# Kernel optimization log

Measured on AMD Instinct MI355X. Metric: run time of the kernel, lower is better.

Reference implementation:

```python
import jax, jax.numpy as jnp
import numpy as np

T, B, D, H = 512, 64, 512, 512

def setup_inputs() -> dict:
    key = jax.random.key(0)
    ks = jax.random.split(key, 14)
    s = 0.02
    inp = {
        "inputs": jax.random.normal(ks[0], (T, B, D), dtype=jnp.float32),
        # gate linears: weight [D+H, H] (transposed torch layout), bias [H]
        "Wf": jax.random.normal(ks[1], (D + H, H), dtype=jnp.float32) * s,
        "bf": jax.random.normal(ks[2], (H,), dtype=jnp.float32) * s,
        "Wi": jax.random.normal(ks[3], (D + H, H), dtype=jnp.float32) * s,
        "bi": jax.random.normal(ks[4], (H,), dtype=jnp.float32) * s,
        "Wg": jax.random.normal(ks[5], (D + H, H), dtype=jnp.float32) * s,
        "bg": jax.random.normal(ks[6], (H,), dtype=jnp.float32) * s,
        "Wo": jax.random.normal(ks[7], (D + H, H), dtype=jnp.float32) * s,
        "bo": jax.random.normal(ks[8], (H,), dtype=jnp.float32) * s,
        # residual linears on hidden state: [H, H], no bias
        "Rf": jax.random.normal(ks[9], (H, H), dtype=jnp.float32) * s,
        "Ri": jax.random.normal(ks[10], (H, H), dtype=jnp.float32) * s,
        "Rg": jax.random.normal(ks[11], (H, H), dtype=jnp.float32) * s,
        "Ro": jax.random.normal(ks[12], (H, H), dtype=jnp.float32) * s,
    }
    return inp


def reference(inputs, Wf, bf, Wi, bi, Wg, bg, Wo, bo, Rf, Ri, Rg, Ro):
    # QLSTM forward (eval mode, gate_dropout inactive). states=None -> zeros.
    batch = inputs.shape[1]
    hidden = Wf.shape[1]
    h0 = jnp.zeros((batch, hidden), dtype=inputs.dtype)
    c0 = jnp.zeros((batch, hidden), dtype=inputs.dtype)

    # Fuse the 4 gate GEMMs into one [D+H, 4H] matmul and the 4 residual
    # GEMMs into one [H, 4H] matmul (same math, fewer launches).
    W4 = jnp.concatenate([Wf, Wi, Wg, Wo], axis=1)   # [D+H, 4H]
    b4 = jnp.concatenate([bf, bi, bg, bo], axis=0)   # [4H]
    R4 = jnp.concatenate([Rf, Ri, Rg, Ro], axis=1)   # [H, 4H]

    def step(carry, x):
        hx, cx = carry
        combined = jnp.concatenate([x, hx], axis=1)            # [B, D+H]
        z = combined @ W4 + b4 + hx @ R4                        # [B, 4H]
        f, i, g, o = jnp.split(z, 4, axis=1)
        f = jax.nn.sigmoid(f)
        i = jax.nn.sigmoid(i)
        g = jnp.tanh(g)
        o = jax.nn.sigmoid(o)
        cx = f * cx + i * g
        hx = o * jnp.tanh(cx)
        return (hx, cx), hx

    (hx, cx), stacked = jax.lax.scan(step, (h0, c0), inputs)
    return stacked, hx, cx
```

## Files before the change

kernel.cpp:

```cpp
#include <hip/hip_runtime.h>
#include <hip/hip_bf16.h>

typedef __attribute__((ext_vector_type(8))) short s16x8;
typedef __attribute__((ext_vector_type(4))) float f32x4;

__device__ __forceinline__ ushort f2bf(float x) {
  __hip_bfloat16 b = __float2bfloat16(x);
  return *reinterpret_cast<ushort*>(&b);
}
__device__ __forceinline__ float bf2f(ushort u) {
  union { unsigned int i; float f; } c; c.i = ((unsigned int)u) << 16; return c.f;
}
__device__ __forceinline__ float sigm_fast(float z) {
  return __builtin_amdgcn_rcpf(1.0f + __builtin_amdgcn_exp2f(z * -1.44269504088896f));
}

__global__ __launch_bounds__(256) void pack_weights(
    const float* __restrict__ Wf, const float* __restrict__ Wi,
    const float* __restrict__ Wg, const float* __restrict__ Wo,
    const float* __restrict__ Rf, const float* __restrict__ Ri,
    const float* __restrict__ Rg, const float* __restrict__ Ro,
    const float* __restrict__ bfp, const float* __restrict__ bip,
    const float* __restrict__ bgp, const float* __restrict__ bop,
    ushort* __restrict__ Wx, ushort* __restrict__ Rs, float* __restrict__ bp)
{
  const int p = blockIdx.x * 8 + (threadIdx.x >> 5);
  const int kk = (threadIdx.x & 31) * 16;
  const int gate = p & 3;
  const int hcol = (p >> 5) * 8 + ((p >> 4) & 1) * 4 + ((p & 15) >> 2);
  const float* W = (gate == 0) ? Wf : (gate == 1) ? Wi : (gate == 2) ? Wg : Wo;
  const float* R = (gate == 0) ? Rf : (gate == 1) ? Ri : (gate == 2) ? Rg : Ro;
  union { ushort u[16]; s16x8 v[2]; } wb, rb;
#pragma unroll
  for (int e = 0; e < 16; ++e) {
    const int k = kk + e;
    wb.u[e] = f2bf(W[(size_t)k * 512 + hcol]);
    rb.u[e] = f2bf(W[(size_t)(512 + k) * 512 + hcol] + R[(size_t)k * 512 + hcol]);
  }
  *(s16x8*)(Wx + (size_t)p * 512 + kk)     = wb.v[0];
  *(s16x8*)(Wx + (size_t)p * 512 + kk + 8) = wb.v[1];
  *(s16x8*)(Rs + (size_t)p * 512 + kk)     = rb.v[0];
  *(s16x8*)(Rs + (size_t)p * 512 + kk + 8) = rb.v[1];
  if ((threadIdx.x & 31) == 0) {
    const float* B = (gate == 0) ? bfp : (gate == 1) ? bip : (gate == 2) ? bgp : bop;
    bp[p] = B[hcol];
  }
}

__global__ __launch_bounds__(512, 1) void fused_kernel(
    const float* __restrict__ x, const ushort* __restrict__ Wx,
    const ushort* __restrict__ Rs, const float* __restrict__ bp,
    const ushort* __restrict__ zxr, ushort* __restrict__ zxw,
    ushort* __restrict__ hbuf, float* __restrict__ csave,
    int* __restrict__ flags, ushort* __restrict__ hsave,
    float* __restrict__ cfinal, int t0, int CH, int zxt0, int do_rec)
{
  __shared__ ushort lds_u[33280];
  const int tid = threadIdx.x;
  const int wid = tid >> 6;
  const int lane = tid & 63;
  const int l15 = lane & 15;
  const int hi = lane >> 4;

  if (blockIdx.x >= 32) {
    if (zxt0 >= 512) return;
    const int zbid = blockIdx.x - 32;
    const int pg = zbid & 15;
    const int ts = zbid >> 4;
    const int mpair = wid >> 2;
    const int np = wid & 3;
    const int q = pg * 4 + np;
    s16x8 Bg[2][16];
#pragma unroll
    for (int nt = 0; nt < 2; ++nt)
#pragma unroll
      for (int kc = 0; kc < 16; ++kc)
        Bg[nt][kc] = *(const s16x8*)(Wx + (size_t)(q * 32 + nt * 16 + l15) * 512 + kc * 32 + hi * 8);
    const int tper = CH >> 3;
    for (int tt = 0; tt < tper; ++tt) {
      const int tl = ts * tper + tt;
      const int t = zxt0 + tl;
      const float4* x4 = (const float4*)(x + (size_t)t * 32768);
#pragma unroll
      for (int j = 0; j < 16; ++j) {
        const int i4 = j * 512 + tid;
        const float4 v = x4[i4];
        const int row = i4 >> 7;
        const int c0 = (i4 & 127) * 4;
        ushort4 u;
        u.x = f2bf(v.x); u.y = f2bf(v.y); u.z = f2bf(v.z); u.w = f2bf(v.w);
        *(ushort4*)(&lds_u[row * 520 + c0]) = u;
      }
      __syncthreads();
#pragma unroll
      for (int a = 0; a < 2; ++a) {
        const int mt = mpair * 2 + a;
        f32x4 a0 = {0.f, 0.f, 0.f, 0.f};
        f32x4 a1 = {0.f, 0.f, 0.f, 0.f};
#pragma unroll
        for (int kc = 0; kc < 16; ++kc) {
          const s16x8 af = *(const s16x8*)(&lds_u[(mt * 16 + l15) * 520 + kc * 32 + hi * 8]);
          a0 = __builtin_amdgcn_mfma_f32_16x16x32_bf16(af, Bg[0][kc], a0, 0, 0, 0);
          a1 = __builtin_amdgcn_mfma_f32_16x16x32_bf16(af, Bg[1][kc], a1, 0, 0, 0);
        }
        union { ushort u[8]; s16x8 v; } ub;
#pragma unroll
        for (int r = 0; r < 4; ++r) { ub.u[r] = f2bf(a0[r]); ub.u[4 + r] = f2bf(a1[r]); }
        *(s16x8*)(zxw + ((((size_t)tl * 4 + mt) * 64 + q) * 64 + lane) * 8) = ub.v;
      }
      __syncthreads();
    }
    return;
  }

  if (!do_rec) return;
  ushort* hsl = lds_u;
  ushort* tbuf = lds_u + 8192;
  const int bid = blockIdx.x;
  const int g = bid >> 3;
  const int mem = bid & 7;
  const int q = mem * 8 + wid;
  const int gate = lane & 3;

  f32x4 Brg[2][16];
#pragma unroll
  for (int nt = 0; nt < 2; ++nt)
#pragma unroll
    for (int kc = 0; kc < 16; ++kc) {
      Brg[nt][kc] = *(const f32x4*)(Rs + (size_t)(q * 32 + nt * 16 + l15) * 512 + kc * 32 + hi * 8);
      asm volatile("" : "+v"(Brg[nt][kc]));
    }
  const float b0 = bp[q * 32 + l15];
  const float b1 = bp[q * 32 + 16 + l15];

  float cst[2][4];
  float* csp = csave + ((size_t)(bid * 8 + wid) * 64 + lane) * 8;
  if (t0 == 0) {
#pragma unroll
    for (int i = 0; i < 2; ++i)
#pragma unroll
      for (int r = 0; r < 4; ++r) cst[i][r] = 0.0f;
  } else {
#pragma unroll
    for (int i = 0; i < 2; ++i)
#pragma unroll
      for (int r = 0; r < 4; ++r) cst[i][r] = csp[i * 4 + r];
  }

  const int srow = hi * 4 + gate;
  const int hcol0 = q * 8 + (l15 >> 2);
  const int crow = tid >> 5;
  const int cbyte = (tid & 31) * 32;
  const int cswz = (crow & 7) << 4;
  const int srcofs = crow * 512 + (cbyte >> 1);
  const int wofs0 = (crow * 1024 + (cbyte ^ cswz)) >> 1;
  const int wofs1 = (crow * 1024 + ((cbyte + 16) ^ cswz)) >> 1;
  const int abase = l15 * 1024 + hi * 16;
  const int aswz = (l15 & 7) << 4;
  int* const myflag = &flags[(g * 8 + mem) * 16];
  const int pollofs = (g * 8 + (lane & 7)) * 16;

  for (int tl = 0; tl < CH; ++tl) {
    const int t = t0 + tl;
    if (tl > 0) {
      asm volatile("s_waitcnt vmcnt(0)" ::: "memory");
      __syncthreads();
      if (tid == 0)
        __hip_atomic_store(myflag, t, __ATOMIC_RELAXED, __HIP_MEMORY_SCOPE_AGENT);
    }
    const s16x8 zv = *(const s16x8*)(zxr + ((((size_t)tl * 4 + g) * 64 + q) * 64 + lane) * 8);
    if (tl > 0) {
      int v;
      do {
        v = __hip_atomic_load(&flags[pollofs], __ATOMIC_RELAXED, __HIP_MEMORY_SCOPE_AGENT);
      } while (!__all(v >= t));
      asm volatile("" ::: "memory");
    }
    const ushort* hs = hbuf + ((size_t)tl * 4 + g) * 8192;
    const s16x8 h0 = *(const s16x8*)(hs + srcofs);
    const s16x8 h1 = *(const s16x8*)(hs + srcofs + 8);
    *(s16x8*)(&hsl[wofs0]) = h0;
    *(s16x8*)(&hsl[wofs1]) = h1;
    __syncthreads();
    f32x4 a0 = {0.f, 0.f, 0.f, 0.f};
    f32x4 a1 = {0.f, 0.f, 0.f, 0.f};
#pragma unroll
    for (int kc = 0; kc < 16; ++kc) {
      const s16x8 af = *(const s16x8*)(&hsl[((abase + kc * 64) ^ aswz) >> 1]);
      a0 = __builtin_amdgcn_mfma_f32_16x16x32_bf16(af, __builtin_bit_cast(s16x8, Brg[0][kc]), a0, 0, 0, 0);
      a1 = __builtin_amdgcn_mfma_f32_16x16x32_bf16(af, __builtin_bit_cast(s16x8, Brg[1][kc]), a1, 0, 0, 0);
    }
    float hv[2], cv[2];
#pragma unroll
    for (int nt = 0; nt < 2; ++nt) {
      float hr[4];
#pragma unroll
      for (int r = 0; r < 4; ++r) {
        float z = (nt ? a1[r] : a0[r]) + bf2f((ushort)zv[nt * 4 + r]) + (nt ? b1 : b0);
        const float zz = (gate == 2) ? z + z : z;
        const float s = sigm_fast(zz);
        const float act = (gate == 2) ? (s + s - 1.0f) : s;
        const int ai = __float_as_int(act);
        const float fv = __int_as_float(__builtin_amdgcn_mov_dpp(ai, 0x00, 0xF, 0xF, true));
        const float iv = __int_as_float(__builtin_amdgcn_mov_dpp(ai, 0x55, 0xF, 0xF, true));
        const float gv = __int_as_float(__builtin_amdgcn_mov_dpp(ai, 0xAA, 0xF, 0xF, true));
        const float ov = __int_as_float(__builtin_amdgcn_mov_dpp(ai, 0xFF, 0xF, 0xF, true));
        const float cn = fmaf(fv, cst[nt][r], iv * gv);
        cst[nt][r] = cn;
        const float s2 = sigm_fast(cn + cn);
        hr[r] = ov * (s2 + s2 - 1.0f);
      }
      hv[nt] = (gate == 0) ? hr[0] : (gate == 1) ? hr[1] : (gate == 2) ? hr[2] : hr[3];
      cv[nt] = (gate == 0) ? cst[nt][0] : (gate == 1) ? cst[nt][1]
             : (gate == 2) ? cst[nt][2] : cst[nt][3];
    }
    const ushort pb0 = f2bf(hv[0]), pb1 = f2bf(hv[1]);
    tbuf[wid * 128 + srow * 8 + (l15 >> 2)]     = pb0;
    tbuf[wid * 128 + srow * 8 + (l15 >> 2) + 4] = pb1;
    asm volatile("s_waitcnt lgkmcnt(0)" ::: "memory");
    __builtin_amdgcn_sched_barrier(0);
    if (tl != CH - 1) {
      if (lane < 16) {
        const unsigned long long* rp = (const unsigned long long*)&tbuf[wid * 128 + lane * 8];
        ushort* dst = hbuf + ((size_t)(tl + 1) * 4 + g) * 8192 + lane * 512 + q * 8;
        __hip_atomic_store((unsigned long long*)dst, rp[0],
                           __ATOMIC_RELAXED, __HIP_MEMORY_SCOPE_AGENT);
        __hip_atomic_store((unsigned long long*)(dst + 4), rp[1],
                           __ATOMIC_RELAXED, __HIP_MEMORY_SCOPE_AGENT);
      }
    } else {
      ushort* hn0 = hbuf + (size_t)g * 8192;
      hn0[srow * 512 + hcol0]     = pb0;
      hn0[srow * 512 + hcol0 + 4] = pb1;
    }
    ushort2 hp; hp.x = pb0; hp.y = pb1;
    *(ushort2*)(hsave + (((size_t)t * 4 + g) * 8 + mem) * 1024 + wid * 128 + lane * 2) = hp;
    if (t == 511) {
      float* cf = cfinal + (((size_t)(g * 8 + mem) * 8 + wid) * 64 + lane) * 2;
      cf[0] = cv[0]; cf[1] = cv[1];
    }
  }
#pragma unroll
  for (int i = 0; i < 2; ++i)
#pragma unroll
    for (int r = 0; r < 4; ++r) csp[i * 4 + r] = cst[i][r];
}

__global__ __launch_bounds__(256) void reorder_kernel(
    const ushort* __restrict__ hsave, const float* __restrict__ cfinal,
    float* __restrict__ dout)
{
  __shared__ ushort lds[8192];
  const int t = blockIdx.x;
  const int g = blockIdx.y;
  const int tid = threadIdx.x;
  const s16x8* src = (const s16x8*)(hsave + ((size_t)t * 4 + g) * 8192);
#pragma unroll
  for (int j = 0; j < 4; ++j) {
    const int i = j * 256 + tid;
    *(s16x8*)(&lds[i * 8]) = src[i];
  }
  __syncthreads();
  const int srow = tid >> 4;
  const int cb = (tid & 15) * 32;
  float buf[32];
#pragma unroll
  for (int cc = 0; cc < 32; ++cc) {
    const int col = cb + cc;
    const int q = col >> 3;
    const int memb = q >> 3;
    const int wd = q & 7;
    const int nt = (col >> 2) & 1;
    const int l15v = ((col & 3) << 2) | (srow & 3);
    const int lanev = ((srow >> 2) << 4) | l15v;
    buf[cc] = bf2f(lds[memb * 1024 + wd * 128 + lanev * 2 + nt]);
  }
  float* o = dout + (size_t)t * 32768 + (size_t)(g * 16 + srow) * 512 + cb;
#pragma unroll
  for (int j = 0; j < 8; ++j) *(float4*)(o + j * 4) = *(const float4*)(&buf[j * 4]);
  if (t == 511) {
    float* oh = dout + (size_t)16777216 + (size_t)(g * 16 + srow) * 512 + cb;
#pragma unroll
    for (int j = 0; j < 8; ++j) *(float4*)(oh + j * 4) = *(const float4*)(&buf[j * 4]);
    float cbuf[32];
#pragma unroll
    for (int cc = 0; cc < 32; ++cc) {
      const int col = cb + cc;
      const int q = col >> 3;
      const int memb = q >> 3;
      const int wd = q & 7;
      const int nt = (col >> 2) & 1;
      const int l15v = ((col & 3) << 2) | (srow & 3);
      const int lanev = ((srow >> 2) << 4) | l15v;
      cbuf[cc] = cfinal[(((size_t)(g * 8 + memb) * 8 + wd) * 64 + lanev) * 2 + nt];
    }
    float* oc = dout + (size_t)16809984 + (size_t)(g * 16 + srow) * 512 + cb;
#pragma unroll
    for (int j = 0; j < 8; ++j) *(float4*)(oc + j * 4) = *(const float4*)(&cbuf[j * 4]);
  }
}

extern "C" void kernel_launch(void* const* d_in, const int* in_sizes, int n_in,
                              void* d_out, int out_size, void* d_ws, size_t ws_size,
                              hipStream_t stream)
{
  const float* x   = (const float*)d_in[0];
  const float* Wf  = (const float*)d_in[1];
  const float* bfp = (const float*)d_in[2];
  const float* Wi  = (const float*)d_in[3];
  const float* bip = (const float*)d_in[4];
  const float* Wg  = (const float*)d_in[5];
  const float* bgp = (const float*)d_in[6];
  const float* Wo  = (const float*)d_in[7];
  const float* bop = (const float*)d_in[8];
  const float* Rf  = (const float*)d_in[9];
  const float* Ri  = (const float*)d_in[10];
  const float* Rg  = (const float*)d_in[11];
  const float* Ro  = (const float*)d_in[12];
  float* dout = (float*)d_out;
  char* ws = (char*)d_ws;

  const size_t o_Wx = 0;
  const size_t o_Rs = 2097152;
  const size_t o_bp = 4194304;
  const size_t o_z0 = o_bp + 8192;

  int CH = 64;
  for (;;) {
    const size_t need = o_z0 + 2 * (size_t)CH * 262144 + (size_t)(CH + 1) * 65536
                      + 524288 + 2048 + 33554432 + 131072;
    if (need <= ws_size || CH <= 8) break;
    CH >>= 1;
  }
  const size_t zsz  = (size_t)CH * 262144;
  const size_t o_z1 = o_z0 + zsz;
  const size_t o_hb = o_z1 + zsz;
  const size_t o_cs = o_hb + (size_t)(CH + 1) * 65536;
  const size_t o_fl = o_cs + 524288;
  const size_t o_hs = o_fl + 2048;
  const size_t o_cf = o_hs + 33554432;

  ushort* Wx   = (ushort*)(ws + o_Wx);
  ushort* Rs   = (ushort*)(ws + o_Rs);
  float*  bp   = (float*)(ws + o_bp);
  ushort* zx0  = (ushort*)(ws + o_z0);
  ushort* zx1  = (ushort*)(ws + o_z1);
  ushort* hb   = (ushort*)(ws + o_hb);
  float*  csv  = (float*)(ws + o_cs);
  int*    fl   = (int*)(ws + o_fl);
  ushort* hsv  = (ushort*)(ws + o_hs);
  float*  cfin = (float*)(ws + o_cf);

  pack_weights<<<256, 256, 0, stream>>>(Wf, Wi, Wg, Wo, Rf, Ri, Rg, Ro,
                                        bfp, bip, bgp, bop, Wx, Rs, bp);
  hipMemsetAsync(hb, 0, 65536, stream);
  hipMemsetAsync(fl, 0, 2048, stream);

  fused_kernel<<<160, 512, 0, stream>>>(x, Wx, Rs, bp, zx1, zx0, hb, csv, fl,
                                        hsv, cfin, 0, CH, 0, 0);
  const int nch = 512 / CH;
  for (int c = 0; c < nch; ++c) {
    const ushort* zr = (c & 1) ? zx1 : zx0;
    ushort* zw       = (c & 1) ? zx0 : zx1;
    fused_kernel<<<160, 512, 0, stream>>>(x, Wx, Rs, bp, zr, zw, hb, csv, fl,
                                          hsv, cfin, c * CH, CH, (c + 1) * CH, 1);
  }
  reorder_kernel<<<dim3(512, 4), 256, 0, stream>>>(hsv, cfin, dout);
}
```

Baseline: 1.722 ms.

## Replace flag-based step barrier with timestamp-tagged packed hidden-state words

Removes the per-step flag store, flag polling and vmcnt drain. Each 64-bit word now carries three bf16 hidden values plus a 16-bit step tag. Consumers spin on the tags of the data they need, and the loads for the next step and the zx values are issued early. This cuts one round trip of cross-block synchronisation on the recurrent critical path. In exchange it packs three values per 8 bytes, which adds traffic overhead, adds a block barrier before publishing, and depends on relaxed-atomic 64-bit stores being seen whole.

```diff
diff --git a/kernel.cpp b/kernel.cpp
--- a/kernel.cpp
+++ b/kernel.cpp
@@ -3,6 +3,7 @@
 
 typedef __attribute__((ext_vector_type(8))) short s16x8;
 typedef __attribute__((ext_vector_type(4))) float f32x4;
+typedef unsigned long long u64;
 
 __device__ __forceinline__ ushort f2bf(float x) {
   __hip_bfloat16 b = __float2bfloat16(x);
@@ -13,6 +14,9 @@
 }
 __device__ __forceinline__ float sigm_fast(float z) {
   return __builtin_amdgcn_rcpf(1.0f + __builtin_amdgcn_exp2f(z * -1.44269504088896f));
+}
+__device__ __forceinline__ u64 aload(const u64* p) {
+  return __hip_atomic_load(p, __ATOMIC_RELAXED, __HIP_MEMORY_SCOPE_AGENT);
 }
 
 __global__ __launch_bounds__(256) void pack_weights(
@@ -51,9 +55,9 @@
     const float* __restrict__ x, const ushort* __restrict__ Wx,
     const ushort* __restrict__ Rs, const float* __restrict__ bp,
     const ushort* __restrict__ zxr, ushort* __restrict__ zxw,
-    ushort* __restrict__ hbuf, float* __restrict__ csave,
-    int* __restrict__ flags, ushort* __restrict__ hsave,
-    float* __restrict__ cfinal, int t0, int CH, int zxt0, int do_rec)
+    u64* __restrict__ hbc, float* __restrict__ csave,
+    ushort* __restrict__ hsave, float* __restrict__ cfinal,
+    int t0, int CH, int zxt0, int do_rec)
 {
   __shared__ ushort lds_u[33280];
   const int tid = threadIdx.x;
@@ -148,39 +152,54 @@
   }
 
   const int srow = hi * 4 + gate;
-  const int hcol0 = q * 8 + (l15 >> 2);
   const int crow = tid >> 5;
+  const int c0 = (tid & 31) * 16;
+  const int memr = c0 >> 6;
+  const int q0c = (crow * 4 + ((c0 & 63) >> 4)) * 6;
   const int cbyte = (tid & 31) * 32;
   const int cswz = (crow & 7) << 4;
-  const int srcofs = crow * 512 + (cbyte >> 1);
   const int wofs0 = (crow * 1024 + (cbyte ^ cswz)) >> 1;
   const int wofs1 = (crow * 1024 + ((cbyte + 16) ^ cswz)) >> 1;
   const int abase = l15 * 1024 + hi * 16;
   const int aswz = (l15 & 7) << 4;
-  int* const myflag = &flags[(g * 8 + mem) * 16];
-  const int pollofs = (g * 8 + (lane & 7)) * 16;
+  const int prow = tid / 24;
+  const int pspan = (tid / 6) & 3;
+  const int pk = tid - (tid / 6) * 6;
+  const int mc0p = pspan * 16 + pk * 3;
+  const int tb0 = (((mc0p) >> 3) & 7) * 128 + prow * 8 + (mc0p & 7);
+  const int mc1p = (mc0p + 1 < (pspan + 1) * 16) ? mc0p + 1 : mc0p;
+  const int mc2p = (mc0p + 2 < (pspan + 1) * 16) ? mc0p + 2 : mc0p;
+  const int tb1 = ((mc1p >> 3) & 7) * 128 + prow * 8 + (mc1p & 7);
+  const int tb2 = ((mc2p >> 3) & 7) * 128 + prow * 8 + (mc2p & 7);
+
+  u64 chv[6];
+  {
+    const u64* cb = hbc + (((size_t)0 * 4 + g) * 8 + memr) * 384 + q0c;
+#pragma unroll
+    for (int i = 0; i < 6; ++i) chv[i] = aload(cb + i);
+  }
+  s16x8 zv = *(const s16x8*)(zxr + ((((size_t)0 * 4 + g) * 64 + q) * 64 + lane) * 8);
 
   for (int tl = 0; tl < CH; ++tl) {
     const int t = t0 + tl;
-    if (tl > 0) {
-      asm volatile("s_waitcnt vmcnt(0)" ::: "memory");
-      __syncthreads();
-      if (tid == 0)
-        __hip_atomic_store(myflag, t, __ATOMIC_RELAXED, __HIP_MEMORY_SCOPE_AGENT);
-    }
-    const s16x8 zv = *(const s16x8*)(zxr + ((((size_t)tl * 4 + g) * 64 + q) * 64 + lane) * 8);
-    if (tl > 0) {
-      int v;
-      do {
-        v = __hip_atomic_load(&flags[pollofs], __ATOMIC_RELAXED, __HIP_MEMORY_SCOPE_AGENT);
-      } while (!__all(v >= t));
-      asm volatile("" ::: "memory");
-    }
-    const ushort* hs = hbuf + ((size_t)tl * 4 + g) * 8192;
-    const s16x8 h0 = *(const s16x8*)(hs + srcofs);
-    const s16x8 h1 = *(const s16x8*)(hs + srcofs + 8);
-    *(s16x8*)(&hsl[wofs0]) = h0;
-    *(s16x8*)(&hsl[wofs1]) = h1;
+    const ushort tau = (ushort)t;
+    {
+      const u64* vb = hbc + (((size_t)tl * 4 + g) * 8 + memr) * 384 + q0c;
+      for (;;) {
+        int ok = 1;
+#pragma unroll
+        for (int i = 0; i < 6; ++i)
+          if ((ushort)(chv[i] >> 48) != tau) { chv[i] = aload(vb + i); ok = 0; }
+        if (ok) break;
+      }
+    }
+    union { ushort u[8]; s16x8 v; } ha, hb2;
+#pragma unroll
+    for (int j = 0; j < 8; ++j)  ha.u[j]      = (ushort)(chv[j / 3] >> (16 * (j % 3)));
+#pragma unroll
+    for (int j = 8; j < 16; ++j) hb2.u[j - 8] = (ushort)(chv[j / 3] >> (16 * (j % 3)));
+    *(s16x8*)(&hsl[wofs0]) = ha.v;
+    *(s16x8*)(&hsl[wofs1]) = hb2.v;
     __syncthreads();
     f32x4 a0 = {0.f, 0.f, 0.f, 0.f};
     f32x4 a1 = {0.f, 0.f, 0.f, 0.f};
@@ -217,27 +236,30 @@
     const ushort pb0 = f2bf(hv[0]), pb1 = f2bf(hv[1]);
     tbuf[wid * 128 + srow * 8 + (l15 >> 2)]     = pb0;
     tbuf[wid * 128 + srow * 8 + (l15 >> 2) + 4] = pb1;
-    asm volatile("s_waitcnt lgkmcnt(0)" ::: "memory");
-    __builtin_amdgcn_sched_barrier(0);
-    if (tl != CH - 1) {
-      if (lane < 16) {
-        const unsigned long long* rp = (const unsigned long long*)&tbuf[wid * 128 + lane * 8];
-        ushort* dst = hbuf + ((size_t)(tl + 1) * 4 + g) * 8192 + lane * 512 + q * 8;
-        __hip_atomic_store((unsigned long long*)dst, rp[0],
-                           __ATOMIC_RELAXED, __HIP_MEMORY_SCOPE_AGENT);
-        __hip_atomic_store((unsigned long long*)(dst + 4), rp[1],
-                           __ATOMIC_RELAXED, __HIP_MEMORY_SCOPE_AGENT);
-      }
-    } else {
-      ushort* hn0 = hbuf + (size_t)g * 8192;
-      hn0[srow * 512 + hcol0]     = pb0;
-      hn0[srow * 512 + hcol0 + 4] = pb1;
-    }
-    ushort2 hp; hp.x = pb0; hp.y = pb1;
-    *(ushort2*)(hsave + (((size_t)t * 4 + g) * 8 + mem) * 1024 + wid * 128 + lane * 2) = hp;
-    if (t == 511) {
-      float* cf = cfinal + (((size_t)(g * 8 + mem) * 8 + wid) * 64 + lane) * 2;
-      cf[0] = cv[0]; cf[1] = cv[1];
+    if (tl + 1 < CH) {
+      const u64* nb = hbc + (((size_t)(tl + 1) * 4 + g) * 8 + memr) * 384 + q0c;
+#pragma unroll
+      for (int i = 0; i < 6; ++i) chv[i] = aload(nb + i);
+      zv = *(const s16x8*)(zxr + ((((size_t)(tl + 1) * 4 + g) * 64 + q) * 64 + lane) * 8);
+    }
+    {
+      ushort2 hp; hp.x = pb0; hp.y = pb1;
+      *(ushort2*)(hsave + (((size_t)t * 4 + g) * 8 + mem) * 1024 + wid * 128 + lane * 2) = hp;
+      if (t == 511) {
+        float* cf = cfinal + (((size_t)(g * 8 + mem) * 8 + wid) * 64 + lane) * 2;
+        cf[0] = cv[0]; cf[1] = cv[1];
+      }
+    }
+    __syncthreads();
+    if (tid < 384) {
+      const ushort v0p = tbuf[tb0];
+      const ushort v1p = tbuf[tb1];
+      const ushort v2p = tbuf[tb2];
+      const u64 pk64 = (u64)v0p | ((u64)v1p << 16) | ((u64)v2p << 32)
+                     | ((u64)(ushort)(t + 1) << 48);
+      const int dsl = (tl + 1 < CH) ? (tl + 1) : 0;
+      __hip_atomic_store(hbc + (((size_t)dsl * 4 + g) * 8 + mem) * 384 + tid, pk64,
+                         __ATOMIC_RELAXED, __HIP_MEMORY_SCOPE_AGENT);
     }
   }
 #pragma unroll
@@ -327,42 +349,41 @@
 
   int CH = 64;
   for (;;) {
-    const size_t need = o_z0 + 2 * (size_t)CH * 262144 + (size_t)(CH + 1) * 65536
-                      + 524288 + 2048 + 33554432 + 131072;
+    const size_t need = o_z0 + 2 * (size_t)CH * 262144
+                      + (size_t)CH * 98304
+                      + 524288 + 33554432 + 131072;
     if (need <= ws_size || CH <= 8) break;
     CH >>= 1;
   }
-  const size_t zsz  = (size_t)CH * 262144;
-  const size_t o_z1 = o_z0 + zsz;
-  const size_t o_hb = o_z1 + zsz;
-  const size_t o_cs = o_hb + (size_t)(CH + 1) * 65536;
-  const size_t o_fl = o_cs + 524288;
-  const size_t o_hs = o_fl + 2048;
-  const size_t o_cf = o_hs + 33554432;
+  const size_t zsz   = (size_t)CH * 262144;
+  const size_t o_z1  = o_z0 + zsz;
+  const size_t o_hbc = o_z1 + zsz;
+  const size_t hbcsz = (size_t)CH * 98304;
+  const size_t o_cs  = o_hbc + hbcsz;
+  const size_t o_hs  = o_cs + 524288;
+  const size_t o_cf  = o_hs + 33554432;
 
   ushort* Wx   = (ushort*)(ws + o_Wx);
   ushort* Rs   = (ushort*)(ws + o_Rs);
   float*  bp   = (float*)(ws + o_bp);
   ushort* zx0  = (ushort*)(ws + o_z0);
   ushort* zx1  = (ushort*)(ws + o_z1);
-  ushort* hb   = (ushort*)(ws + o_hb);
+  u64*    hbc  = (u64*)(ws + o_hbc);
   float*  csv  = (float*)(ws + o_cs);
-  int*    fl   = (int*)(ws + o_fl);
   ushort* hsv  = (ushort*)(ws + o_hs);
   float*  cfin = (float*)(ws + o_cf);
 
   pack_weights<<<256, 256, 0, stream>>>(Wf, Wi, Wg, Wo, Rf, Ri, Rg, Ro,
                                         bfp, bip, bgp, bop, Wx, Rs, bp);
-  hipMemsetAsync(hb, 0, 65536, stream);
-  hipMemsetAsync(fl, 0, 2048, stream);
-
-  fused_kernel<<<160, 512, 0, stream>>>(x, Wx, Rs, bp, zx1, zx0, hb, csv, fl,
+  hipMemsetAsync(hbc, 0, hbcsz, stream);
+
+  fused_kernel<<<160, 512, 0, stream>>>(x, Wx, Rs, bp, zx1, zx0, hbc, csv,
                                         hsv, cfin, 0, CH, 0, 0);
   const int nch = 512 / CH;
   for (int c = 0; c < nch; ++c) {
     const ushort* zr = (c & 1) ? zx1 : zx0;
     ushort* zw       = (c & 1) ? zx0 : zx1;
-    fused_kernel<<<160, 512, 0, stream>>>(x, Wx, Rs, bp, zr, zw, hb, csv, fl,
+    fused_kernel<<<160, 512, 0, stream>>>(x, Wx, Rs, bp, zr, zw, hbc, csv,
                                           hsv, cfin, c * CH, CH, (c + 1) * CH, 1);
   }
   reorder_kernel<<<dim3(512, 4), 256, 0, stream>>>(hsv, cfin, dout);
```

Result: slower. 2.362 ms (+37.1%).
